# Performance work log

Hardware: AMD Instinct MI355X
Metric: run time of the kernel (lower is better)

The kernel has to match this reference:

```python
import jax, jax.numpy as jnp
import numpy as np

V, E, HID, T = 50000, 256, 512, 12   # vocab, embed dim, lstm hidden (bi total), tagset size
START, STOP = 10, 11
L = 2048                              # sentence length
H = HID // 2                          # per-direction hidden
NEG = -10000.0


def setup_inputs():
    key = jax.random.key(0)
    ks = jax.random.split(key, 13)
    s = 0.05
    sentence = jax.random.randint(ks[0], (L,), 0, V)
    embed = jax.random.normal(ks[1], (V, E), jnp.float32) * s
    w_ih_f = jax.random.normal(ks[2], (4 * H, E), jnp.float32) * s
    w_hh_f = jax.random.normal(ks[3], (4 * H, H), jnp.float32) * s
    b_ih_f = jax.random.normal(ks[4], (4 * H,), jnp.float32) * s
    b_hh_f = jax.random.normal(ks[5], (4 * H,), jnp.float32) * s
    w_ih_b = jax.random.normal(ks[6], (4 * H, E), jnp.float32) * s
    w_hh_b = jax.random.normal(ks[7], (4 * H, H), jnp.float32) * s
    b_ih_b = jax.random.normal(ks[8], (4 * H,), jnp.float32) * s
    b_hh_b = jax.random.normal(ks[9], (4 * H,), jnp.float32) * s
    w_out = jax.random.normal(ks[10], (T, HID), jnp.float32) * s
    b_out = jax.random.normal(ks[11], (T,), jnp.float32) * s
    transitions = jax.random.normal(ks[12], (T, T), jnp.float32)
    transitions = transitions.at[START, :].set(NEG).at[:, STOP].set(NEG)
    return dict(sentence=sentence, embed=embed,
                w_ih_f=w_ih_f, w_hh_f=w_hh_f, b_ih_f=b_ih_f, b_hh_f=b_hh_f,
                w_ih_b=w_ih_b, w_hh_b=w_hh_b, b_ih_b=b_ih_b, b_hh_b=b_hh_b,
                w_out=w_out, b_out=b_out, transitions=transitions)


def _lstm_dir(x, w_ih, w_hh, b, reverse):
    # x: [L, E] -> hs: [L, H]; PyTorch gate order i, f, g, o
    xg = x @ w_ih.T + b  # [L, 4H] precomputed input contribution

    def step(carry, xg_t):
        h, c = carry
        g = xg_t + h @ w_hh.T
        i, f, gg, o = jnp.split(g, 4)
        i, f, o = jax.nn.sigmoid(i), jax.nn.sigmoid(f), jax.nn.sigmoid(o)
        c = f * c + i * jnp.tanh(gg)
        h = o * jnp.tanh(c)
        return (h, c), h

    hdim = w_hh.shape[1]
    init = (jnp.zeros((hdim,), x.dtype), jnp.zeros((hdim,), x.dtype))
    _, hs = jax.lax.scan(step, init, xg, reverse=reverse)
    return hs


def _lstm_feats(sentence, embed, w_ih_f, w_hh_f, b_ih_f, b_hh_f,
                w_ih_b, w_hh_b, b_ih_b, b_hh_b, w_out, b_out):
    x = embed[sentence]                                        # [L, E]
    hf = _lstm_dir(x, w_ih_f, w_hh_f, b_ih_f + b_hh_f, False)  # [L, H]
    hb = _lstm_dir(x, w_ih_b, w_hh_b, b_ih_b + b_hh_b, True)   # [L, H]
    h = jnp.concatenate([hf, hb], axis=-1)                     # [L, 2H]
    return h @ w_out.T + b_out                                 # [L, T]


def reference(sentence, embed, w_ih_f, w_hh_f, b_ih_f, b_hh_f,
              w_ih_b, w_hh_b, b_ih_b, b_hh_b, w_out, b_out, transitions):
    feats = _lstm_feats(sentence, embed, w_ih_f, w_hh_f, b_ih_f, b_hh_f,
                        w_ih_b, w_hh_b, b_ih_b, b_hh_b, w_out, b_out)

    # Viterbi DP vectorized over tags, scanned over time
    init_v = jnp.full((T,), NEG, feats.dtype).at[START].set(0.0)

    def vstep(v, feat):
        scores = transitions + v[None, :]        # [next_tag, prev_tag]
        bp = jnp.argmax(scores, axis=1)          # best previous tag per next tag
        v_new = jnp.max(scores, axis=1) + feat
        return v_new, bp

    v, bps = jax.lax.scan(vstep, init_v, feats)  # bps: [L, T]
    terminal = v + transitions[STOP]
    best = jnp.argmax(terminal)
    path_score = terminal[best]

    def btrack(tag, bp):
        return bp[tag], tag

    _, best_path = jax.lax.scan(btrack, best, bps, reverse=True)  # [L] tags
    return path_score, best_path
```

## Files before the change

### kernel.cpp

```cpp
#include <hip/hip_runtime.h>

#define LSEQ 2048
#define TAGS 12

typedef _Float16 half2v __attribute__((ext_vector_type(2)));
typedef unsigned long long u64;

__device__ __forceinline__ float sigm(float x){ return 1.0f/(1.0f+__expf(-x)); }
__device__ __forceinline__ float tanh_fast(float x){ return 1.0f - 2.0f/(1.0f+__expf(2.0f*x)); }
__device__ __forceinline__ half2v pack2(float a, float b){
  half2v r; r.x=(_Float16)a; r.y=(_Float16)b; return r;
}

__global__ void xg_kernel(
    const int* sent, const float* embed,
    const float* w_ih_f, const float* b_ih_f, const float* b_hh_f,
    const float* w_ih_b, const float* b_ih_b, const float* b_hh_b,
    float* xg, u64* ex)
{
  __shared__ float x_sh[8][256];
  int tid = threadIdx.x;
  if (blockIdx.x == 0){
    #pragma unroll
    for (int i=0;i<4;++i) ex[tid + 256*i] = 0ull;
  }
  int t0 = blockIdx.x * 8;
  for (int i=0;i<8;++i){
    int idx = sent[t0+i];
    x_sh[i][tid] = embed[(size_t)idx*256 + tid];
  }
  __syncthreads();
  for (int ri=0; ri<8; ++ri){
    int r = ri*256 + tid;
    int d = r >> 10;
    int row = r & 1023;
    const float* wr = (d ? w_ih_b : w_ih_f) + (size_t)row*256;
    const float* bi = d ? b_ih_b : b_ih_f;
    const float* bh = d ? b_hh_b : b_hh_f;
    float acc[8];
    #pragma unroll
    for (int i=0;i<8;++i) acc[i]=0.f;
    for (int k0=0;k0<256;k0+=4){
      float4 p = *(const float4*)(wr + k0);
      #pragma unroll
      for (int i=0;i<8;++i){
        acc[i] += p.x*x_sh[i][k0] + p.y*x_sh[i][k0+1]
                + p.z*x_sh[i][k0+2] + p.w*x_sh[i][k0+3];
      }
    }
    float bias = bi[row] + bh[row];
    #pragma unroll
    for (int i=0;i<8;++i)
      xg[((size_t)d*LSEQ + (size_t)(t0+i))*1024 + row] = acc[i] + bias;
  }
}

__global__ __launch_bounds__(256,1) void lstm_rec(
    const float* __restrict__ w_hh_f, const float* __restrict__ w_hh_b,
    const float* __restrict__ xg, unsigned short* __restrict__ hstH,
    u64* __restrict__ ex)
{
  int blk = blockIdx.x;
  int d = blk & 7;
  if (d > 1) return;
  int q = blk >> 3;
  int qa = (q+1)&3, qb = (q+2)&3, qc = (q+3)&3;

  int tid = threadIdx.x;
  int g = tid >> 6, l = tid & 63;
  int m = l & 31;
  int row = g*256 + 64*q + l;
  const float* W = d ? w_hh_b : w_hh_f;
  const float* xgd = xg + (size_t)d*LSEQ*1024;
  unsigned short* hd = hstH + (size_t)d*LSEQ*256;
  u64* exd = ex + (size_t)d*256;

  __shared__ float gate_sh[256];
  __shared__ __align__(16) unsigned h2rem[96];

  half2v w[128];
  {
    const float* p0 = W + (size_t)row*256 + 64*q;
    const float* p1 = W + (size_t)row*256 + 64*qa;
    const float* p2 = W + (size_t)row*256 + 64*qb;
    const float* p3 = W + (size_t)row*256 + 64*qc;
    #pragma unroll
    for (int k0=0;k0<16;++k0){
      float4 a = *(const float4*)(p0+4*k0);
      w[2*k0]      = pack2(a.x,a.y);  w[2*k0+1]    = pack2(a.z,a.w);
      float4 b = *(const float4*)(p1+4*k0);
      w[32+2*k0]   = pack2(b.x,b.y);  w[32+2*k0+1] = pack2(b.z,b.w);
      float4 cc= *(const float4*)(p2+4*k0);
      w[64+2*k0]   = pack2(cc.x,cc.y); w[64+2*k0+1] = pack2(cc.z,cc.w);
      float4 e = *(const float4*)(p3+4*k0);
      w[96+2*k0]   = pack2(e.x,e.y);  w[96+2*k0+1] = pack2(e.z,e.w);
    }
  }
  if (tid < 96) h2rem[tid] = 0u;
  float c0 = 0.f, c1 = 0.f;
  unsigned hl = 0u;

  int pollj = tid - 64;
  int pollpeer = (q + 1 + (pollj>>5)) & 3;
  int pollslot = 32*pollpeer + (pollj & 31);
  bool isPoller = (tid >= 64) && (tid < 160);
  __syncthreads();

  int tf = d ? (LSEQ-1) : 0;
  float xg0 = xgd[(size_t)tf*1024 + row];

  for (int s=0;s<LSEQ;++s){
    u64 v0 = 0ull;
    bool poll = (s > 0) && isPoller;
    if (poll)
      v0 = __hip_atomic_load(&exd[((s&1)<<7) + pollslot],
                             __ATOMIC_RELAXED, __HIP_MEMORY_SCOPE_AGENT);
    float a0=xg0, a1=0.f, a2=0.f, a3=0.f;
    #pragma unroll
    for (int k=0;k<32;k+=4){
      unsigned p0v = __builtin_amdgcn_readlane(hl,k);
      unsigned p1v = __builtin_amdgcn_readlane(hl,k+1);
      unsigned p2v = __builtin_amdgcn_readlane(hl,k+2);
      unsigned p3v = __builtin_amdgcn_readlane(hl,k+3);
      a0 = __builtin_amdgcn_fdot2(__builtin_bit_cast(half2v,p0v), w[k],   a0, false);
      a1 = __builtin_amdgcn_fdot2(__builtin_bit_cast(half2v,p1v), w[k+1], a1, false);
      a2 = __builtin_amdgcn_fdot2(__builtin_bit_cast(half2v,p2v), w[k+2], a2, false);
      a3 = __builtin_amdgcn_fdot2(__builtin_bit_cast(half2v,p3v), w[k+3], a3, false);
    }
    if (poll){
      u64 v = v0;
      while ((unsigned)(v>>32) != (unsigned)s)
        v = __hip_atomic_load(&exd[((s&1)<<7) + pollslot],
                              __ATOMIC_RELAXED, __HIP_MEMORY_SCOPE_AGENT);
      h2rem[pollj] = (unsigned)v;
    }
    float nxg = 0.f;
    if (s+1 < LSEQ){
      int tn = d ? (LSEQ-2-s) : (s+1);
      nxg = xgd[(size_t)tn*1024 + row];
    }
    __syncthreads();
    #pragma unroll
    for (int j=0;j<24;++j){
      uint4 hv = *(const uint4*)&h2rem[4*j];
      a0 = __builtin_amdgcn_fdot2(__builtin_bit_cast(half2v,hv.x), w[32+4*j],   a0, false);
      a1 = __builtin_amdgcn_fdot2(__builtin_bit_cast(half2v,hv.y), w[32+4*j+1], a1, false);
      a2 = __builtin_amdgcn_fdot2(__builtin_bit_cast(half2v,hv.z), w[32+4*j+2], a2, false);
      a3 = __builtin_amdgcn_fdot2(__builtin_bit_cast(half2v,hv.w), w[32+4*j+3], a3, false);
    }
    float pre = (a0+a1) + (a2+a3);
    float act = (g==2) ? tanh_fast(pre) : sigm(pre);
    gate_sh[tid] = act;
    xg0 = nxg;
    __syncthreads();
    {
      float2 gi = *(const float2*)&gate_sh[      2*m];
      float2 gf = *(const float2*)&gate_sh[ 64 + 2*m];
      float2 gg = *(const float2*)&gate_sh[128 + 2*m];
      float2 go = *(const float2*)&gate_sh[192 + 2*m];
      c0 = gf.x*c0 + gi.x*gg.x;
      c1 = gf.y*c1 + gi.y*gg.y;
      float h0 = go.x * tanh_fast(c0);
      float h1 = go.y * tanh_fast(c1);
      hl = __builtin_bit_cast(unsigned, pack2(h0,h1));
    }
    if (tid < 32){
      if (s+1 < LSEQ)
        __hip_atomic_store(&exd[(((s+1)&1)<<7) + 32*q + tid],
                           ((u64)(unsigned)(s+1) << 32) | (u64)hl,
                           __ATOMIC_RELAXED, __HIP_MEMORY_SCOPE_AGENT);
      int tp = d ? (LSEQ-1-s) : s;
      *(unsigned*)&hd[(size_t)tp*256 + 64*q + 2*tid] = hl;
    }
  }
}

__global__ void feats_kernel(
    const unsigned short* hstH, const float* w_out, const float* b_out,
    float* feats)
{
  __shared__ float w_sh[12*520];
  __shared__ float h_sh[16*520];
  const _Float16* hf = (const _Float16*)hstH;
  int tid=threadIdx.x;
  int t0=blockIdx.x*16;
  for (int i=tid;i<12*512;i+=256){ int tag=i>>9,k=i&511; w_sh[tag*520+k]=w_out[i]; }
  for (int i=tid;i<16*512;i+=256){
    int tt=i>>9,k=i&511;
    float v = (k<256)? (float)hf[(size_t)(t0+tt)*256+k]
                     : (float)hf[(size_t)(LSEQ+t0+tt)*256 + (k-256)];
    h_sh[tt*520+k]=v;
  }
  __syncthreads();
  if (tid<192){
    int tt=tid/12, tag=tid%12;
    const float* wr=&w_sh[tag*520];
    const float* hr=&h_sh[tt*520];
    float acc=b_out[tag];
    for (int k=0;k<512;k+=4){
      float4 a=*(const float4*)(wr+k);
      float4 b=*(const float4*)(hr+k);
      acc += a.x*b.x+a.y*b.y+a.z*b.z+a.w*b.w;
    }
    feats[(size_t)(t0+tt)*12+tag]=acc;
  }
}

__global__ void BiLSTM_CRF_14405320311361_kernel(
    const float* feats, const float* trans, float* outp)
{
  __shared__ float fsh[LSEQ*12];
  __shared__ unsigned char bps[LSEQ*12];
  __shared__ float term_sh[16];
  __shared__ int ibuf[66];
  __shared__ unsigned char fmap[64*12];
  int tid = threadIdx.x;
  for (int i=tid; i<LSEQ*12/4; i+=256)
    *(float4*)&fsh[4*i] = *(const float4*)&feats[4*i];
  __syncthreads();

  int lane = tid & 63;
  int fl = (lane<12) ? lane : 0;
  float vn = 0.f;
  if (tid < 64){
    float tr[12];
    #pragma unroll
    for (int p=0;p<12;++p) tr[p] = trans[fl*12+p];
    vn = (lane==10) ? 0.f : -10000.f;
    float fa = fsh[fl];
    float fb = fsh[12+fl];
    for (int t=0;t<LSEQ;++t){
      unsigned vu = __float_as_uint(vn);
      float best; int bp; float sc;
      best = tr[0] + __uint_as_float(__builtin_amdgcn_readlane(vu,0)); bp = 0;
      sc = tr[1]  + __uint_as_float(__builtin_amdgcn_readlane(vu,1));  if(sc>best){best=sc;bp=1;}
      sc = tr[2]  + __uint_as_float(__builtin_amdgcn_readlane(vu,2));  if(sc>best){best=sc;bp=2;}
      sc = tr[3]  + __uint_as_float(__builtin_amdgcn_readlane(vu,3));  if(sc>best){best=sc;bp=3;}
      sc = tr[4]  + __uint_as_float(__builtin_amdgcn_readlane(vu,4));  if(sc>best){best=sc;bp=4;}
      sc = tr[5]  + __uint_as_float(__builtin_amdgcn_readlane(vu,5));  if(sc>best){best=sc;bp=5;}
      sc = tr[6]  + __uint_as_float(__builtin_amdgcn_readlane(vu,6));  if(sc>best){best=sc;bp=6;}
      sc = tr[7]  + __uint_as_float(__builtin_amdgcn_readlane(vu,7));  if(sc>best){best=sc;bp=7;}
      sc = tr[8]  + __uint_as_float(__builtin_amdgcn_readlane(vu,8));  if(sc>best){best=sc;bp=8;}
      sc = tr[9]  + __uint_as_float(__builtin_amdgcn_readlane(vu,9));  if(sc>best){best=sc;bp=9;}
      sc = tr[10] + __uint_as_float(__builtin_amdgcn_readlane(vu,10)); if(sc>best){best=sc;bp=10;}
      sc = tr[11] + __uint_as_float(__builtin_amdgcn_readlane(vu,11)); if(sc>best){best=sc;bp=11;}
      vn = best + fa;
      fa = fb;
      if (t+2 < LSEQ) fb = fsh[(t+2)*12+fl];
      if (lane<12) bps[t*12+lane] = (unsigned char)bp;
    }
  }
  if (tid < 12) term_sh[tid] = vn + trans[11*12+tid];
  __syncthreads();
  if (tid == 0){
    float bs=term_sh[0]; int bt=0;
    for (int p=1;p<12;++p){ if (term_sh[p]>bs){bs=term_sh[p];bt=p;} }
    outp[0] = bs;
    ibuf[64] = bt;
  }
  __syncthreads();
  if (tid < 64){
    int b = tid;
    int f[12];
    int thi = b*32+31;
    #pragma unroll
    for (int x=0;x<12;++x) f[x] = bps[thi*12+x];
    for (int t=thi-1; t>=b*32; --t){
      int base = t*12;
      #pragma unroll
      for (int x=0;x<12;++x) f[x] = bps[base + f[x]];
    }
    #pragma unroll
    for (int x=0;x<12;++x) fmap[b*12+x] = (unsigned char)f[x];
  }
  __syncthreads();
  if (tid == 0){
    int tag = ibuf[64];
    for (int b=63;b>=0;--b){ ibuf[b]=tag; tag = fmap[b*12+tag]; }
  }
  __syncthreads();
  if (tid < 64){
    int b = tid;
    int tag = ibuf[b];
    for (int t=b*32+31; t>=b*32; --t){
      outp[1+t] = (float)tag;
      tag = bps[t*12+tag];
    }
  }
}

extern "C" void kernel_launch(void* const* d_in, const int* in_sizes, int n_in,
                              void* d_out, int out_size, void* d_ws, size_t ws_size,
                              hipStream_t stream) {
  const int*   sent   = (const int*)d_in[0];
  const float* embed  = (const float*)d_in[1];
  const float* w_ih_f = (const float*)d_in[2];
  const float* w_hh_f = (const float*)d_in[3];
  const float* b_ih_f = (const float*)d_in[4];
  const float* b_hh_f = (const float*)d_in[5];
  const float* w_ih_b = (const float*)d_in[6];
  const float* w_hh_b = (const float*)d_in[7];
  const float* b_ih_b = (const float*)d_in[8];
  const float* b_hh_b = (const float*)d_in[9];
  const float* w_out  = (const float*)d_in[10];
  const float* b_out  = (const float*)d_in[11];
  const float* trans  = (const float*)d_in[12];

  float* xg = (float*)d_ws;
  unsigned short* hstH = (unsigned short*)(xg + (size_t)2*LSEQ*1024);
  u64* ex = (u64*)(hstH + (size_t)2*LSEQ*256);
  float* feats = (float*)(ex + 1024);
  float* outp  = (float*)d_out;

  xg_kernel<<<dim3(LSEQ/8), dim3(256), 0, stream>>>(
      sent, embed, w_ih_f, b_ih_f, b_hh_f, w_ih_b, b_ih_b, b_hh_b, xg, ex);
  lstm_rec<<<dim3(32), dim3(256), 0, stream>>>(w_hh_f, w_hh_b, xg, hstH, ex);
  feats_kernel<<<dim3(LSEQ/16), dim3(256), 0, stream>>>(hstH, w_out, b_out, feats);
  BiLSTM_CRF_14405320311361_kernel<<<dim3(1), dim3(256), 0, stream>>>(feats, trans, outp);
}
```

Measured before the change: 3.551 ms.

## Place recurrent LSTM workgroups on one XCD and exchange hidden state via L2

Launches 256 workgroups and, using the hardware XCC id register plus atomics, picks the first XCD to arrive and assigns the 8 recurrent roles only to workgroups on that die. All cooperating workgroups then share one L2. Per-step hidden-state exchange uses raw global store/load (sc0) that bypass device-scope coherence, with a fallback to agent-scope atomics on a mirror copy after several failed polls. This is meant to cut cross-die latency in the per-timestep handshake. It relies on undocumented hwreg encoding and on cache-coherence assumptions, and it could deadlock or stall if 8 blocks are not co-resident on that XCD.

```diff
diff --git a/kernel.cpp b/kernel.cpp
--- a/kernel.cpp
+++ b/kernel.cpp
@@ -12,17 +12,28 @@
   half2v r; r.x=(_Float16)a; r.y=(_Float16)b; return r;
 }
 
+__device__ __forceinline__ void st_l2(u64* p, u64 v){
+  asm volatile("global_store_dwordx2 %0, %1, off" :: "v"(p), "v"(v) : "memory");
+}
+__device__ __forceinline__ u64 ld_l2(const u64* p){
+  u64 v;
+  asm volatile("global_load_dwordx2 %0, %1, off sc0\n\ts_waitcnt vmcnt(0)"
+               : "=v"(v) : "v"(p) : "memory");
+  return v;
+}
+
 __global__ void xg_kernel(
     const int* sent, const float* embed,
     const float* w_ih_f, const float* b_ih_f, const float* b_hh_f,
     const float* w_ih_b, const float* b_ih_b, const float* b_hh_b,
-    float* xg, u64* ex)
+    float* xg, u64* ex, unsigned* cnt)
 {
   __shared__ float x_sh[8][256];
   int tid = threadIdx.x;
   if (blockIdx.x == 0){
     #pragma unroll
     for (int i=0;i<4;++i) ex[tid + 256*i] = 0ull;
+    if (tid < 2) cnt[tid] = 0u;
   }
   int t0 = blockIdx.x * 8;
   for (int i=0;i<8;++i){
@@ -58,12 +69,27 @@
 __global__ __launch_bounds__(256,1) void lstm_rec(
     const float* __restrict__ w_hh_f, const float* __restrict__ w_hh_b,
     const float* __restrict__ xg, unsigned short* __restrict__ hstH,
-    u64* __restrict__ ex)
+    u64* __restrict__ ex, unsigned* __restrict__ cnt)
 {
-  int blk = blockIdx.x;
-  int d = blk & 7;
-  if (d > 1) return;
-  int q = blk >> 3;
+  __shared__ int role_sh;
+  if (threadIdx.x == 0){
+    unsigned xcc;
+    asm volatile("s_getreg_b32 %0, hwreg(20, 0, 32)" : "=s"(xcc));
+    unsigned my = (xcc & 7u) + 1u;
+    unsigned prev = atomicCAS(&cnt[0], 0u, my);
+    unsigned leader = prev ? prev : my;
+    int role = -1;
+    if (my == leader){
+      unsigned r = atomicAdd(&cnt[1], 1u);
+      if (r < 8u) role = (int)r;
+    }
+    role_sh = role;
+  }
+  __syncthreads();
+  int role = role_sh;
+  if (role < 0) return;
+  int d = role >> 2;
+  int q = role & 3;
   int qa = (q+1)&3, qb = (q+2)&3, qc = (q+3)&3;
 
   int tid = threadIdx.x;
@@ -112,9 +138,8 @@
   for (int s=0;s<LSEQ;++s){
     u64 v0 = 0ull;
     bool poll = (s > 0) && isPoller;
-    if (poll)
-      v0 = __hip_atomic_load(&exd[((s&1)<<7) + pollslot],
-                             __ATOMIC_RELAXED, __HIP_MEMORY_SCOPE_AGENT);
+    const u64* fp = &exd[((s&1)<<7) + pollslot];
+    if (poll) v0 = ld_l2(fp);
     float a0=xg0, a1=0.f, a2=0.f, a3=0.f;
     #pragma unroll
     for (int k=0;k<32;k+=4){
@@ -129,9 +154,12 @@
     }
     if (poll){
       u64 v = v0;
-      while ((unsigned)(v>>32) != (unsigned)s)
-        v = __hip_atomic_load(&exd[((s&1)<<7) + pollslot],
-                              __ATOMIC_RELAXED, __HIP_MEMORY_SCOPE_AGENT);
+      int tries = 0;
+      while ((unsigned)(v>>32) != (unsigned)s){
+        ++tries;
+        if (tries < 10) v = ld_l2(fp);
+        else v = __hip_atomic_load(fp + 512, __ATOMIC_RELAXED, __HIP_MEMORY_SCOPE_AGENT);
+      }
       h2rem[pollj] = (unsigned)v;
     }
     float nxg = 0.f;
@@ -165,10 +193,13 @@
       hl = __builtin_bit_cast(unsigned, pack2(h0,h1));
     }
     if (tid < 32){
-      if (s+1 < LSEQ)
-        __hip_atomic_store(&exd[(((s+1)&1)<<7) + 32*q + tid],
-                           ((u64)(unsigned)(s+1) << 32) | (u64)hl,
+      if (s+1 < LSEQ){
+        u64 pk = ((u64)(unsigned)(s+1) << 32) | (u64)hl;
+        u64* p = &exd[(((s+1)&1)<<7) + 32*q + tid];
+        st_l2(p, pk);
+        __hip_atomic_store(p + 512, pk,
                            __ATOMIC_RELAXED, __HIP_MEMORY_SCOPE_AGENT);
+      }
       int tp = d ? (LSEQ-1-s) : s;
       *(unsigned*)&hd[(size_t)tp*256 + 64*q + 2*tid] = hl;
     }
@@ -309,12 +340,13 @@
   float* xg = (float*)d_ws;
   unsigned short* hstH = (unsigned short*)(xg + (size_t)2*LSEQ*1024);
   u64* ex = (u64*)(hstH + (size_t)2*LSEQ*256);
-  float* feats = (float*)(ex + 1024);
+  unsigned* cnt = (unsigned*)(ex + 1024);
+  float* feats = (float*)(cnt + 16);
   float* outp  = (float*)d_out;
 
   xg_kernel<<<dim3(LSEQ/8), dim3(256), 0, stream>>>(
-      sent, embed, w_ih_f, b_ih_f, b_hh_f, w_ih_b, b_ih_b, b_hh_b, xg, ex);
-  lstm_rec<<<dim3(32), dim3(256), 0, stream>>>(w_hh_f, w_hh_b, xg, hstH, ex);
+      sent, embed, w_ih_f, b_ih_f, b_hh_f, w_ih_b, b_ih_b, b_hh_b, xg, ex, cnt);
+  lstm_rec<<<dim3(256), dim3(256), 0, stream>>>(w_hh_f, w_hh_b, xg, hstH, ex, cnt);
   feats_kernel<<<dim3(LSEQ/16), dim3(256), 0, stream>>>(hstH, w_out, b_out, feats);
   BiLSTM_CRF_14405320311361_kernel<<<dim3(1), dim3(256), 0, stream>>>(feats, trans, outp);
 }
```

Result: slower. 6.202 ms (+74.6%).
